# Kernel tuning notes

Hardware: AMD Instinct MI355X
Metric: run time of the kernel (lower is better)

The kernel has to match this reference:

```python
import jax, jax.numpy as jnp
import numpy as np

N_NODES = 100000
N_EDGES = 3200000
N_GRAPHS = 1024
D = 64
STEPS_PROP = 6
STEPS_S2S = 6


def setup_inputs() -> dict:
    key = jax.random.key(0)
    ks = jax.random.split(key, 16)
    inp = {}
    inp['x'] = jax.random.normal(ks[0], (N_NODES, 15), dtype=jnp.float32)
    inp['edge_index'] = jax.random.randint(ks[1], (2, N_EDGES), 0, N_NODES, dtype=jnp.int64 if jax.config.jax_enable_x64 else jnp.int32)
    inp['batch'] = jnp.sort(jax.random.randint(ks[2], (N_NODES,), 0, N_GRAPHS, dtype=jnp.int64 if jax.config.jax_enable_x64 else jnp.int32))
    s = 0.1
    inp['W0'] = jax.random.normal(ks[3], (15, D), dtype=jnp.float32) * s
    inp['b0'] = jax.random.normal(ks[4], (D,), dtype=jnp.float32) * s
    inp['Wc'] = jax.random.normal(ks[5], (D, D), dtype=jnp.float32) * s
    inp['bc'] = jax.random.normal(ks[6], (D,), dtype=jnp.float32) * s
    inp['Wih'] = jax.random.normal(ks[7], (4 * D, 2 * D), dtype=jnp.float32) * s
    inp['Whh'] = jax.random.normal(ks[8], (4 * D, D), dtype=jnp.float32) * s
    inp['bih'] = jax.random.normal(ks[9], (4 * D,), dtype=jnp.float32) * s
    inp['bhh'] = jax.random.normal(ks[10], (4 * D,), dtype=jnp.float32) * s
    inp['W1'] = jax.random.normal(ks[11], (2 * D, D), dtype=jnp.float32) * s
    inp['b1'] = jax.random.normal(ks[12], (D,), dtype=jnp.float32) * s
    inp['W2'] = jax.random.normal(ks[13], (D, 12), dtype=jnp.float32) * s
    inp['b2'] = jax.random.normal(ks[14], (12,), dtype=jnp.float32) * s
    return inp


def _gcn_forward(x, edge_index, batch, W0, b0, Wc, bc, Wih, Whh, bih, bhh, W1, b1, W2, b2):
    N = x.shape[0]
    # GCNConv normalization with self-loops (PyG semantics): A_hat = D^-1/2 (A+I) D^-1/2
    loops = jnp.arange(N, dtype=edge_index.dtype)
    row = jnp.concatenate([edge_index[0], loops])  # source
    col = jnp.concatenate([edge_index[1], loops])  # target
    deg = jax.ops.segment_sum(jnp.ones_like(col, dtype=x.dtype), col, num_segments=N)
    dinv = jnp.where(deg > 0, jax.lax.rsqrt(jnp.maximum(deg, 1e-30)), 0.0)
    norm = dinv[row] * dinv[col]  # [E+N]

    out = jax.nn.relu(x @ W0 + b0)  # [N, D]
    for _ in range(STEPS_PROP):
        h = out @ Wc  # transform first
        msg = h[row] * norm[:, None]  # gather along edges
        out = jax.nn.relu(jax.ops.segment_sum(msg, col, num_segments=N) + bc)

    # Set2Set pooling
    B = N_GRAPHS
    d = out.shape[1]
    h_l = jnp.zeros((B, d), dtype=out.dtype)
    c_l = jnp.zeros((B, d), dtype=out.dtype)
    q_star = jnp.zeros((B, 2 * d), dtype=out.dtype)
    for _ in range(STEPS_S2S):
        gates = q_star @ Wih.T + h_l @ Whh.T + bih + bhh  # [B, 4d]
        i_g, f_g, g_g, o_g = jnp.split(gates, 4, axis=1)
        c_l = jax.nn.sigmoid(f_g) * c_l + jax.nn.sigmoid(i_g) * jnp.tanh(g_g)
        h_l = jax.nn.sigmoid(o_g) * jnp.tanh(c_l)
        q = h_l  # [B, d]
        e = jnp.sum(out * q[batch], axis=-1)  # [N]
        m = jax.ops.segment_max(e, batch, num_segments=B)
        a_num = jnp.exp(e - m[batch])
        denom = jax.ops.segment_sum(a_num, batch, num_segments=B)
        a = a_num / denom[batch]
        r = jax.ops.segment_sum(a[:, None] * out, batch, num_segments=B)  # [B, d]
        q_star = jnp.concatenate([q, r], axis=-1)

    y = jax.nn.relu(q_star @ W1 + b1)
    return y @ W2 + b2  # [B, 12]


def reference(x, edge_index, batch, W0, b0, Wc, bc, Wih, Whh, bih, bhh, W1, b1, W2, b2):
    return _gcn_forward(x, edge_index, batch, W0, b0, Wc, bc, Wih, Whh, bih, bhh, W1, b1, W2, b2)
```

## Files before the change

kernel.cpp:

```cpp
#include <hip/hip_runtime.h>
#include <hip/hip_fp16.h>
#include <math.h>

#define ND 64
constexpr int BKT_SHIFT = 9;
constexpr int BKT_MASK = (1 << BKT_SHIFT) - 1;
constexpr int BCUR_PAD = 16;
constexpr int STG_TILE = 8192;
constexpr int S2S_CAP = 192;

__device__ __forceinline__ float sigmoidf_(float x){ return 1.f/(1.f+__expf(-x)); }
__device__ __forceinline__ __half2 h2lo(uint2 v){ return *reinterpret_cast<__half2*>(&v.x); }
__device__ __forceinline__ __half2 h2hi(uint2 v){ return *reinterpret_cast<__half2*>(&v.y); }
__device__ __forceinline__ __half2 shxor_h2(__half2 h, int off){
  unsigned u = *reinterpret_cast<unsigned*>(&h);
  u = __shfl_xor(u, off, 64);
  return *reinterpret_cast<__half2*>(&u);
}

__global__ void k_bhist(const int* __restrict__ col, int* __restrict__ bgcnt,
                        int E, int NBK){
  __shared__ int lhist[512];
  int t0 = blockIdx.x * STG_TILE;
  int t1 = t0 + STG_TILE; if (t1 > E) t1 = E;
  for (int i = threadIdx.x; i < NBK; i += 256) lhist[i] = 0;
  __syncthreads();
  for (int i = t0 + threadIdx.x; i < t1; i += 256)
    atomicAdd(&lhist[col[i] >> BKT_SHIFT], 1);
  __syncthreads();
  for (int i = threadIdx.x; i < NBK; i += 256)
    if (lhist[i] > 0) atomicAdd(&bgcnt[i], lhist[i]);
}

__global__ void k_bscan(const int* __restrict__ bgcnt, int* __restrict__ bstart,
                        int* __restrict__ rowptr, int NBK, int E, int N){
  __shared__ int tmp[256];
  int t = threadIdx.x;
  int v = (t < NBK) ? bgcnt[t] : 0;
  tmp[t] = v; __syncthreads();
  for (int off=1; off<256; off<<=1){
    int u = (t>=off) ? tmp[t-off] : 0;
    __syncthreads();
    tmp[t] += u;
    __syncthreads();
  }
  if (t <= NBK) bstart[t] = (t==0) ? 0 : tmp[t-1];
  if (t == 0) rowptr[N] = E;
}

__global__ void k_bcinit(const int* __restrict__ bstart, int* __restrict__ bcur, int NBK){
  int b = blockIdx.x*blockDim.x + threadIdx.x;
  if (b < NBK) bcur[b*BCUR_PAD] = bstart[b];
}

__global__ void k_stage2(const int* __restrict__ row, const int* __restrict__ col,
                         int* __restrict__ bcur, unsigned* __restrict__ pairs,
                         int E, int NBK){
  __shared__ int lhist[512];
  __shared__ int lbase[512];
  int t0 = blockIdx.x * STG_TILE;
  int t1 = t0 + STG_TILE; if (t1 > E) t1 = E;
  for (int i = threadIdx.x; i < NBK; i += 256) lhist[i] = 0;
  __syncthreads();
  for (int i = t0 + threadIdx.x; i < t1; i += 256)
    atomicAdd(&lhist[col[i] >> BKT_SHIFT], 1);
  __syncthreads();
  for (int i = threadIdx.x; i < NBK; i += 256){
    int c = lhist[i];
    lbase[i] = (c > 0) ? atomicAdd(&bcur[i*BCUR_PAD], c) : 0;
    lhist[i] = 0;
  }
  __syncthreads();
  for (int i = t0 + threadIdx.x; i < t1; i += 256){
    int d = col[i];
    int b = d >> BKT_SHIFT;
    int pos = lbase[b] + atomicAdd(&lhist[b], 1);
    pairs[pos] = ((unsigned)row[i] << BKT_SHIFT) | (unsigned)(d & BKT_MASK);
  }
}

__global__ void k_place(const unsigned* __restrict__ pairs, const int* __restrict__ bstart,
                        int* __restrict__ rowptr, float* __restrict__ dinv,
                        int* __restrict__ csr, int N){
  __shared__ int h[1 << BKT_SHIFT];
  __shared__ int excl[1 << BKT_SHIFT];
  __shared__ int tsum[256];
  int b = blockIdx.x;
  int base = b << BKT_SHIFT;
  int nend = base + (1 << BKT_SHIFT); if (nend > N) nend = N;
  int cnt = nend - base;
  int t = threadIdx.x;
  int s = bstart[b], e = bstart[b+1];

  h[2*t] = 0; h[2*t+1] = 0;
  __syncthreads();
  for (int i = s + t; i < e; i += 256)
    atomicAdd(&h[pairs[i] & BKT_MASK], 1);
  __syncthreads();
  int a0 = h[2*t], a1 = h[2*t+1];
  tsum[t] = a0 + a1;
  __syncthreads();
  for (int off=1; off<256; off<<=1){
    int u = (t>=off) ? tsum[t-off] : 0;
    __syncthreads();
    tsum[t] += u;
    __syncthreads();
  }
  int base0 = (t==0) ? 0 : tsum[t-1];
  excl[2*t]   = base0;
  excl[2*t+1] = base0 + a0;
  __syncthreads();
  for (int c = t; c < cnt; c += 256){
    int deg = h[c];
    rowptr[base + c] = s + excl[c];
    dinv[base + c] = rsqrtf((float)(deg + 1));
  }
  __syncthreads();
  for (int c = t; c < cnt; c += 256) h[c] = s + excl[c];
  __syncthreads();
  for (int i = s + t; i < e; i += 256){
    unsigned p = pairs[i];
    int pos = atomicAdd(&h[p & BKT_MASK], 1);
    csr[pos] = (int)(p >> BKT_SHIFT);
  }
}

__global__ void k_input(const float* __restrict__ x, const float* __restrict__ W0,
                        const float* __restrict__ b0, const float* __restrict__ dinv,
                        __half* __restrict__ s, int N){
  __shared__ float w0s[15*ND];
  __shared__ float b0s[ND];
  int tid = threadIdx.x;
  for (int i=tid; i<15*ND; i+=256) w0s[i] = W0[i];
  if (tid < ND) b0s[tid] = b0[tid];
  __syncthreads();
  int node = blockIdx.x*4 + (tid>>6);
  int f = tid & 63;
  if (node < N){
    float acc = b0s[f];
    const float* xr = x + (size_t)node*15;
    #pragma unroll
    for (int k=0;k<15;k++) acc += xr[k]*w0s[k*ND+f];
    s[(size_t)node*ND+f] = __float2half_rn(dinv[node]*fmaxf(acc, 0.f));
  }
}

__global__ void k_prop(const __half* __restrict__ sbuf, const int* __restrict__ rowptr,
                       const int* __restrict__ csr, const float* __restrict__ dinv,
                       const float* __restrict__ Wc, const float* __restrict__ bc,
                       __half* __restrict__ s_new, __half* __restrict__ outh,
                       int N, int wout){
  __shared__ float wcs[ND*ND];
  __shared__ float xs[16][ND];
  __shared__ float bcs[ND];
  const uint2* g8 = (const uint2*)sbuf;
  int tid = threadIdx.x;
  for (int i=tid; i<ND*ND; i+=256) wcs[i] = Wc[i];
  if (tid < ND) bcs[tid] = bc[tid];
  int nb = blockIdx.x*16;
  int wv = tid>>6, lane = tid&63;
  int grp = lane>>4, li = lane&15;

  for (int q=0; q<4; ++q){
    int node = nb + wv*4 + q;
    float val = 0.f;
    if (node < N){
      int s = rowptr[node], e = rowptr[node+1];
      __half2 z = __float2half2_rn(0.f);
      __half2 a0x=z,a0y=z, a1x=z,a1y=z, a2x=z,a2y=z, a3x=z,a3y=z;
      int i = s;
      for (; i + 16 <= e; i += 16){
        int s0 = csr[i +  0 + grp];
        int s1 = csr[i +  4 + grp];
        int s2 = csr[i +  8 + grp];
        int s3 = csr[i + 12 + grp];
        uint2 v0 = g8[(size_t)s0*16 + li];
        uint2 v1 = g8[(size_t)s1*16 + li];
        uint2 v2 = g8[(size_t)s2*16 + li];
        uint2 v3 = g8[(size_t)s3*16 + li];
        a0x = __hadd2(a0x, h2lo(v0)); a0y = __hadd2(a0y, h2hi(v0));
        a1x = __hadd2(a1x, h2lo(v1)); a1y = __hadd2(a1y, h2hi(v1));
        a2x = __hadd2(a2x, h2lo(v2)); a2y = __hadd2(a2y, h2hi(v2));
        a3x = __hadd2(a3x, h2lo(v3)); a3y = __hadd2(a3y, h2hi(v3));
      }
      for (; i + 4 <= e; i += 4){
        int s0 = csr[i + grp];
        uint2 v0 = g8[(size_t)s0*16 + li];
        a0x = __hadd2(a0x, h2lo(v0)); a0y = __hadd2(a0y, h2hi(v0));
      }
      int r = e - i;
      if (grp < r){
        int s0 = csr[i + grp];
        uint2 v0 = g8[(size_t)s0*16 + li];
        a1x = __hadd2(a1x, h2lo(v0)); a1y = __hadd2(a1y, h2hi(v0));
      }
      __half2 sxh = __hadd2(__hadd2(a0x,a1x), __hadd2(a2x,a3x));
      __half2 syh = __hadd2(__hadd2(a0y,a1y), __hadd2(a2y,a3y));
      sxh = __hadd2(sxh, shxor_h2(sxh, 16));
      syh = __hadd2(syh, shxor_h2(syh, 16));
      sxh = __hadd2(sxh, shxor_h2(sxh, 32));
      syh = __hadd2(syh, shxor_h2(syh, 32));
      uint2 sv = g8[(size_t)node*16 + li];
      sxh = __hadd2(sxh, h2lo(sv));
      syh = __hadd2(syh, h2hi(sv));
      val = (grp==0) ? __half2float(__low2half(sxh))
          : (grp==1) ? __half2float(__high2half(sxh))
          : (grp==2) ? __half2float(__low2half(syh))
          :            __half2float(__high2half(syh));
    }
    xs[wv*4+q][4*li+grp] = val;
  }
  __syncthreads();

  int f = tid&63, nq = tid>>6;
  float acc0=0.f, acc1=0.f, acc2=0.f, acc3=0.f;
  #pragma unroll 16
  for (int k=0;k<ND;k++){
    float w = wcs[k*ND+f];
    acc0 += w*xs[nq*4+0][k];
    acc1 += w*xs[nq*4+1][k];
    acc2 += w*xs[nq*4+2][k];
    acc3 += w*xs[nq*4+3][k];
  }
  int n0 = nb + nq*4;
  float bcf = bcs[f];
  #pragma unroll
  for (int j=0; j<4; ++j){
    int node = n0 + j;
    if (node < N){
      float a = (j==0)?acc0:(j==1)?acc1:(j==2)?acc2:acc3;
      float dn = dinv[node];
      float r = fmaxf(dn*a + bcf, 0.f);
      if (wout) outh[(size_t)node*ND+f] = __float2half_rn(r);
      else      s_new[(size_t)node*ND+f] = __float2half_rn(dn*r);
    }
  }
}

__global__ void k_goff(const int* __restrict__ batch, int* __restrict__ goff, int N, int B){
  int i = blockIdx.x*blockDim.x + threadIdx.x;
  if (i >= N) return;
  int b = batch[i];
  if (i == 0){ for (int g2=0; g2<=b; ++g2) goff[g2]=0; }
  else {
    int bp = batch[i-1];
    for (int g2=bp+1; g2<=b; ++g2) goff[g2]=i;
  }
  if (i == N-1){ for (int g2=b+1; g2<=B; ++g2) goff[g2]=N; }
}

__global__ void k_wprep(const float* __restrict__ Wih, const float* __restrict__ Whh,
                        const float* __restrict__ bih, const float* __restrict__ bhh,
                        float* __restrict__ WcombT, float* __restrict__ WrT,
                        float* __restrict__ bsum){
  int k = blockIdx.x;
  int j = threadIdx.x;
  WcombT[k*256 + j] = Wih[(size_t)j*128 + k] + Whh[(size_t)j*64 + k];
  WrT  [k*256 + j] = Wih[(size_t)j*128 + 64 + k];
  if (k == 0) bsum[j] = bih[j] + bhh[j];
}

__global__ void k_s2s(const __half* __restrict__ nodef, const int* __restrict__ goff,
                      const float* __restrict__ WcombT, const float* __restrict__ WrT,
                      const float* __restrict__ bsum,
                      const float* __restrict__ W1, const float* __restrict__ b1,
                      const float* __restrict__ W2, const float* __restrict__ b2,
                      float* __restrict__ outy, int B){
  __shared__ float qsr[128];
  __shared__ float clr[64];
  __shared__ float gat[256];
  __shared__ float redm[16], redd[16];
  __shared__ float redr[16][64];
  __shared__ float yy[64];
  extern __shared__ uint2 snode[];
  int tid = threadIdx.x;
  int g = blockIdx.x;
  if (g >= B) return;
  if (tid < 128) qsr[tid] = 0.f;
  if (tid < 64)  clr[tid] = 0.f;
  int lane = tid&63, wv = tid>>6;
  int grp = lane>>4, li = lane&15;
  int gidx = wv*4 + grp;
  int s = goff[g], e = goff[g+1];
  int cnt = e - s;
  const uint2* nf = (const uint2*)nodef;
  bool lds_ok = (cnt <= S2S_CAP);
  if (lds_ok){
    for (int i = tid; i < cnt*16; i += 256){
      int n = i >> 4, c = i & 15;
      snode[n*17 + c] = nf[(size_t)(s+n)*16 + c];
    }
  }
  __syncthreads();

  for (int step=0; step<6; ++step){
    {
      float a0 = bsum[tid], a1 = 0.f;
      for (int k=0; k<64; k+=2){
        a0 += WcombT[(k  )*256+tid]*qsr[k  ] + WrT[(k  )*256+tid]*qsr[64+k  ];
        a1 += WcombT[(k+1)*256+tid]*qsr[k+1] + WrT[(k+1)*256+tid]*qsr[64+k+1];
      }
      gat[tid] = a0 + a1;
    }
    __syncthreads();
    if (tid < 64){
      float ig = sigmoidf_(gat[tid]);
      float fg = sigmoidf_(gat[64+tid]);
      float gv = tanhf(gat[128+tid]);
      float og = sigmoidf_(gat[192+tid]);
      float c = fg*clr[tid] + ig*gv;
      float h = og*tanhf(c);
      clr[tid] = c;
      qsr[tid] = h;
    }
    __syncthreads();
    {
      float4 q4 = *(const float4*)&qsr[4*li];
      float m = -3.0e38f, denom = 0.f;
      float r0=0.f, r1=0.f, r2=0.f, r3=0.f;
      if (lds_ok){
        for (int n = gidx; n < cnt; n += 16){
          uint2 v = snode[n*17 + li];
          float2 flo = __half22float2(h2lo(v));
          float2 fhi = __half22float2(h2hi(v));
          float p = flo.x*q4.x + flo.y*q4.y + fhi.x*q4.z + fhi.y*q4.w;
          p += __shfl_xor(p, 1, 64);
          p += __shfl_xor(p, 2, 64);
          p += __shfl_xor(p, 4, 64);
          p += __shfl_xor(p, 8, 64);
          if (p > m){
            float sc = __expf(m - p);
            denom *= sc; r0 *= sc; r1 *= sc; r2 *= sc; r3 *= sc;
            m = p;
          }
          float w = __expf(p - m);
          denom += w;
          r0 += w*flo.x; r1 += w*flo.y; r2 += w*fhi.x; r3 += w*fhi.y;
        }
      } else {
        for (int n = s + gidx; n < e; n += 16){
          uint2 v = nf[(size_t)n*16 + li];
          float2 flo = __half22float2(h2lo(v));
          float2 fhi = __half22float2(h2hi(v));
          float p = flo.x*q4.x + flo.y*q4.y + fhi.x*q4.z + fhi.y*q4.w;
          p += __shfl_xor(p, 1, 64);
          p += __shfl_xor(p, 2, 64);
          p += __shfl_xor(p, 4, 64);
          p += __shfl_xor(p, 8, 64);
          if (p > m){
            float sc = __expf(m - p);
            denom *= sc; r0 *= sc; r1 *= sc; r2 *= sc; r3 *= sc;
            m = p;
          }
          float w = __expf(p - m);
          denom += w;
          r0 += w*flo.x; r1 += w*flo.y; r2 += w*fhi.x; r3 += w*fhi.y;
        }
      }
      if (li == 0){ redm[gidx] = m; redd[gidx] = denom; }
      redr[gidx][4*li+0] = r0;
      redr[gidx][4*li+1] = r1;
      redr[gidx][4*li+2] = r2;
      redr[gidx][4*li+3] = r3;
    }
    __syncthreads();
    if (tid < 64){
      float mm = -3.0e38f;
      #pragma unroll
      for (int k=0;k<16;k++) mm = fmaxf(mm, redm[k]);
      float dt = 0.f, rs = 0.f;
      #pragma unroll
      for (int k=0;k<16;k++){
        float sc = __expf(redm[k] - mm);
        dt += redd[k]*sc;
        rs += redr[k][tid]*sc;
      }
      qsr[64+tid] = (dt > 0.f) ? rs/dt : 0.f;
    }
    __syncthreads();
  }
  if (tid < 64){
    float acc = b1[tid];
    for (int k=0;k<128;k++) acc += qsr[k]*W1[k*64+tid];
    yy[tid] = fmaxf(acc, 0.f);
  }
  __syncthreads();
  if (tid < 12){
    float a2 = b2[tid];
    for (int k=0;k<64;k++) a2 += yy[k]*W2[k*12+tid];
    outy[(size_t)g*12+tid] = a2;
  }
}

extern "C" void kernel_launch(void* const* d_in, const int* in_sizes, int n_in,
                              void* d_out, int out_size, void* d_ws, size_t ws_size,
                              hipStream_t stream){
  const float* x    = (const float*)d_in[0];
  const int*   ei   = (const int*)d_in[1];
  const int*   batch= (const int*)d_in[2];
  const float* W0   = (const float*)d_in[3];
  const float* b0   = (const float*)d_in[4];
  const float* Wc   = (const float*)d_in[5];
  const float* bc   = (const float*)d_in[6];
  const float* Wih  = (const float*)d_in[7];
  const float* Whh  = (const float*)d_in[8];
  const float* bih  = (const float*)d_in[9];
  const float* bhh  = (const float*)d_in[10];
  const float* W1   = (const float*)d_in[11];
  const float* b1   = (const float*)d_in[12];
  const float* W2   = (const float*)d_in[13];
  const float* b2   = (const float*)d_in[14];
  float* yout = (float*)d_out;

  const int N = in_sizes[0]/15;
  const int E = in_sizes[1]/2;
  const int B = out_size/12;
  const int NBK = (N + (1<<BKT_SHIFT) - 1) >> BKT_SHIFT;
  const int* row = ei;
  const int* col = ei + E;

  char* ws = (char*)d_ws;
  size_t off = 0;
  auto alloc = [&](size_t bytes)->void*{
    void* p = ws + off; off = (off + bytes + 255) & ~(size_t)255; return p;
  };
  int*      bgcnt   = (int*)     alloc((size_t)(NBK+1)*4);
  int*      bstart  = (int*)     alloc((size_t)(NBK+1)*4);
  int*      bcur    = (int*)     alloc((size_t)NBK*BCUR_PAD*4);
  int*      rowptr  = (int*)     alloc((size_t)(N+1)*4);
  unsigned* pairs   = (unsigned*)alloc((size_t)E*4);
  int*      csr     = (int*)     alloc((size_t)E*4);
  float*    dinv    = (float*)   alloc((size_t)N*4);
  __half*   nodef   = (__half*)  alloc((size_t)N*ND*2);
  __half*   s_a     = (__half*)  alloc((size_t)N*ND*2);
  __half*   s_b     = (__half*)  alloc((size_t)N*ND*2);
  int*      goff    = (int*)     alloc((size_t)(B+1)*4);
  float*    WcombT  = (float*)   alloc(64*256*4);
  float*    WrT     = (float*)   alloc(64*256*4);
  float*    bsum    = (float*)   alloc(256*4);
  (void)ws_size; (void)n_in;

  hipMemsetAsync(bgcnt, 0, (size_t)(NBK+1)*4, stream);

  int nstg = (E + STG_TILE - 1)/STG_TILE;
  k_bhist <<<nstg, 256, 0, stream>>>(col, bgcnt, E, NBK);
  k_bscan <<<1, 256, 0, stream>>>(bgcnt, bstart, rowptr, NBK, E, N);
  k_bcinit<<<(NBK+255)/256, 256, 0, stream>>>(bstart, bcur, NBK);
  k_stage2<<<nstg, 256, 0, stream>>>(row, col, bcur, pairs, E, NBK);
  k_place <<<NBK, 256, 0, stream>>>(pairs, bstart, rowptr, dinv, csr, N);

  k_input<<<(N+3)/4, 256, 0, stream>>>(x, W0, b0, dinv, s_a, N);
  __half* scur = s_a; __half* snxt = s_b;
  for (int s6=0; s6<6; ++s6){
    k_prop<<<(N+15)/16, 256, 0, stream>>>(scur, rowptr, csr, dinv,
                                          Wc, bc, snxt, nodef, N, (s6==5)?1:0);
    __half* t = scur; scur = snxt; snxt = t;
  }

  k_goff<<<(N+255)/256, 256, 0, stream>>>(batch, goff, N, B);
  k_wprep<<<64, 256, 0, stream>>>(Wih, Whh, bih, bhh, WcombT, WrT, bsum);
  size_t s2s_lds = (size_t)S2S_CAP*17*sizeof(uint2);
  k_s2s<<<B, 256, s2s_lds, stream>>>(nodef, goff, WcombT, WrT, bsum,
                                     W1, b1, W2, b2, yout, B);
}
```

Baseline: 854.6 us.

## Batch four graphs per Set2Set block with fp16 LSTM weights staged in LDS

The Set2Set kernel now handles four graphs per 256-thread block, with one wavefront per graph for the attention pass. It stages the LSTM weights, prepacked as half2, into LDS once per block so that each weight element is reused across four graphs. The LDS node cache shrinks to 144 nodes per graph. Weight traffic and block count go down, but gate weights lose fp16 precision. Each graph gets only one wave for attention, larger graphs spill to the global path, and the high LDS use may cut occupancy.

```diff
diff --git a/kernel.cpp b/kernel.cpp
--- a/kernel.cpp
+++ b/kernel.cpp
@@ -7,7 +7,7 @@
 constexpr int BKT_MASK = (1 << BKT_SHIFT) - 1;
 constexpr int BCUR_PAD = 16;
 constexpr int STG_TILE = 8192;
-constexpr int S2S_CAP = 192;
+constexpr int S2S_CAP = 144;
 
 __device__ __forceinline__ float sigmoidf_(float x){ return 1.f/(1.f+__expf(-x)); }
 __device__ __forceinline__ __half2 h2lo(uint2 v){ return *reinterpret_cast<__half2*>(&v.x); }
@@ -251,76 +251,108 @@
 
 __global__ void k_wprep(const float* __restrict__ Wih, const float* __restrict__ Whh,
                         const float* __restrict__ bih, const float* __restrict__ bhh,
-                        float* __restrict__ WcombT, float* __restrict__ WrT,
+                        unsigned* __restrict__ WC2, unsigned* __restrict__ WR2,
                         float* __restrict__ bsum){
-  int k = blockIdx.x;
-  int j = threadIdx.x;
-  WcombT[k*256 + j] = Wih[(size_t)j*128 + k] + Whh[(size_t)j*64 + k];
-  WrT  [k*256 + j] = Wih[(size_t)j*128 + 64 + k];
-  if (k == 0) bsum[j] = bih[j] + bhh[j];
+  int k2 = blockIdx.x;
+  int j  = threadIdx.x;
+  int k = 2*k2;
+  float c0 = Wih[(size_t)j*128 + k]     + Whh[(size_t)j*64 + k];
+  float c1 = Wih[(size_t)j*128 + k + 1] + Whh[(size_t)j*64 + k + 1];
+  float r0 = Wih[(size_t)j*128 + 64 + k];
+  float r1 = Wih[(size_t)j*128 + 64 + k + 1];
+  __half2 hc = __halves2half2(__float2half_rn(c0), __float2half_rn(c1));
+  __half2 hr = __halves2half2(__float2half_rn(r0), __float2half_rn(r1));
+  WC2[k2*256 + j] = *reinterpret_cast<unsigned*>(&hc);
+  WR2[k2*256 + j] = *reinterpret_cast<unsigned*>(&hr);
+  if (k2 == 0) bsum[j] = bih[j] + bhh[j];
 }
 
 __global__ void k_s2s(const __half* __restrict__ nodef, const int* __restrict__ goff,
-                      const float* __restrict__ WcombT, const float* __restrict__ WrT,
+                      const unsigned* __restrict__ WC2g, const unsigned* __restrict__ WR2g,
                       const float* __restrict__ bsum,
                       const float* __restrict__ W1, const float* __restrict__ b1,
                       const float* __restrict__ W2, const float* __restrict__ b2,
                       float* __restrict__ outy, int B){
-  __shared__ float qsr[128];
-  __shared__ float clr[64];
-  __shared__ float gat[256];
-  __shared__ float redm[16], redd[16];
-  __shared__ float redr[16][64];
-  __shared__ float yy[64];
-  extern __shared__ uint2 snode[];
+  __shared__ unsigned lwc[32*256];
+  __shared__ unsigned lwr[32*256];
+  __shared__ float qsr[4][128];
+  __shared__ float clr[4][64];
+  __shared__ float gat[4][256];
+  __shared__ float redm[4][4], redd[4][4];
+  __shared__ float redr[4][4][64];
+  __shared__ float yy[4][64];
+  __shared__ uint2 snode[4][S2S_CAP*17];
+
   int tid = threadIdx.x;
-  int g = blockIdx.x;
-  if (g >= B) return;
-  if (tid < 128) qsr[tid] = 0.f;
-  if (tid < 64)  clr[tid] = 0.f;
+  int g0 = blockIdx.x*4;
   int lane = tid&63, wv = tid>>6;
   int grp = lane>>4, li = lane&15;
-  int gidx = wv*4 + grp;
-  int s = goff[g], e = goff[g+1];
-  int cnt = e - s;
+
+  for (int i=tid; i<32*256; i+=256){ lwc[i] = WC2g[i]; lwr[i] = WR2g[i]; }
+  for (int i=tid; i<4*128; i+=256) qsr[i>>7][i&127] = 0.f;
+  if (tid < 256){ clr[tid>>6][tid&63] = 0.f; }
+
+  int mygraph = g0 + wv;
+  int s = 0, cnt = 0;
   const uint2* nf = (const uint2*)nodef;
-  bool lds_ok = (cnt <= S2S_CAP);
-  if (lds_ok){
-    for (int i = tid; i < cnt*16; i += 256){
-      int n = i >> 4, c = i & 15;
-      snode[n*17 + c] = nf[(size_t)(s+n)*16 + c];
-    }
-  }
+  bool lds_ok = false;
+  if (mygraph < B){
+    s = goff[mygraph];
+    cnt = goff[mygraph+1] - s;
+    lds_ok = (cnt <= S2S_CAP);
+    if (lds_ok){
+      for (int i = lane; i < cnt*16; i += 64){
+        int n = i >> 4, c = i & 15;
+        snode[wv][n*17 + c] = nf[(size_t)(s+n)*16 + c];
+      }
+    }
+  }
+  float bsv = bsum[tid];
   __syncthreads();
 
   for (int step=0; step<6; ++step){
     {
-      float a0 = bsum[tid], a1 = 0.f;
-      for (int k=0; k<64; k+=2){
-        a0 += WcombT[(k  )*256+tid]*qsr[k  ] + WrT[(k  )*256+tid]*qsr[64+k  ];
-        a1 += WcombT[(k+1)*256+tid]*qsr[k+1] + WrT[(k+1)*256+tid]*qsr[64+k+1];
-      }
-      gat[tid] = a0 + a1;
-    }
-    __syncthreads();
-    if (tid < 64){
-      float ig = sigmoidf_(gat[tid]);
-      float fg = sigmoidf_(gat[64+tid]);
-      float gv = tanhf(gat[128+tid]);
-      float og = sigmoidf_(gat[192+tid]);
-      float c = fg*clr[tid] + ig*gv;
+      float a0=bsv, a1=bsv, a2=bsv, a3=bsv;
+      for (int k2=0; k2<32; ++k2){
+        unsigned uc = lwc[k2*256 + tid];
+        unsigned ur = lwr[k2*256 + tid];
+        float2 wc = __half22float2(*reinterpret_cast<__half2*>(&uc));
+        float2 wr = __half22float2(*reinterpret_cast<__half2*>(&ur));
+        float2 h0 = *(const float2*)&qsr[0][2*k2];
+        float2 h1 = *(const float2*)&qsr[1][2*k2];
+        float2 h2 = *(const float2*)&qsr[2][2*k2];
+        float2 h3 = *(const float2*)&qsr[3][2*k2];
+        float2 r0 = *(const float2*)&qsr[0][64+2*k2];
+        float2 r1 = *(const float2*)&qsr[1][64+2*k2];
+        float2 r2 = *(const float2*)&qsr[2][64+2*k2];
+        float2 r3 = *(const float2*)&qsr[3][64+2*k2];
+        a0 += wc.x*h0.x + wc.y*h0.y + wr.x*r0.x + wr.y*r0.y;
+        a1 += wc.x*h1.x + wc.y*h1.y + wr.x*r1.x + wr.y*r1.y;
+        a2 += wc.x*h2.x + wc.y*h2.y + wr.x*r2.x + wr.y*r2.y;
+        a3 += wc.x*h3.x + wc.y*h3.y + wr.x*r3.x + wr.y*r3.y;
+      }
+      gat[0][tid]=a0; gat[1][tid]=a1; gat[2][tid]=a2; gat[3][tid]=a3;
+    }
+    __syncthreads();
+    {
+      int gg = tid>>6, d = tid&63;
+      float ig = sigmoidf_(gat[gg][d]);
+      float fg = sigmoidf_(gat[gg][64+d]);
+      float gv = tanhf(gat[gg][128+d]);
+      float og = sigmoidf_(gat[gg][192+d]);
+      float c = fg*clr[gg][d] + ig*gv;
       float h = og*tanhf(c);
-      clr[tid] = c;
-      qsr[tid] = h;
+      clr[gg][d] = c;
+      qsr[gg][d] = h;
     }
     __syncthreads();
     {
-      float4 q4 = *(const float4*)&qsr[4*li];
+      float4 q4 = *(const float4*)&qsr[wv][4*li];
       float m = -3.0e38f, denom = 0.f;
       float r0=0.f, r1=0.f, r2=0.f, r3=0.f;
       if (lds_ok){
-        for (int n = gidx; n < cnt; n += 16){
-          uint2 v = snode[n*17 + li];
+        for (int n = grp; n < cnt; n += 4){
+          uint2 v = snode[wv][n*17 + li];
           float2 flo = __half22float2(h2lo(v));
           float2 fhi = __half22float2(h2hi(v));
           float p = flo.x*q4.x + flo.y*q4.y + fhi.x*q4.z + fhi.y*q4.w;
@@ -337,9 +369,9 @@
           denom += w;
           r0 += w*flo.x; r1 += w*flo.y; r2 += w*fhi.x; r3 += w*fhi.y;
         }
-      } else {
-        for (int n = s + gidx; n < e; n += 16){
-          uint2 v = nf[(size_t)n*16 + li];
+      } else if (mygraph < B){
+        for (int n = grp; n < cnt; n += 4){
+          uint2 v = nf[(size_t)(s+n)*16 + li];
           float2 flo = __half22float2(h2lo(v));
           float2 fhi = __half22float2(h2hi(v));
           float p = flo.x*q4.x + flo.y*q4.y + fhi.x*q4.z + fhi.y*q4.w;
@@ -357,38 +389,38 @@
           r0 += w*flo.x; r1 += w*flo.y; r2 += w*fhi.x; r3 += w*fhi.y;
         }
       }
-      if (li == 0){ redm[gidx] = m; redd[gidx] = denom; }
-      redr[gidx][4*li+0] = r0;
-      redr[gidx][4*li+1] = r1;
-      redr[gidx][4*li+2] = r2;
-      redr[gidx][4*li+3] = r3;
-    }
-    __syncthreads();
-    if (tid < 64){
-      float mm = -3.0e38f;
-      #pragma unroll
-      for (int k=0;k<16;k++) mm = fmaxf(mm, redm[k]);
-      float dt = 0.f, rs = 0.f;
-      #pragma unroll
-      for (int k=0;k<16;k++){
-        float sc = __expf(redm[k] - mm);
-        dt += redd[k]*sc;
-        rs += redr[k][tid]*sc;
-      }
-      qsr[64+tid] = (dt > 0.f) ? rs/dt : 0.f;
-    }
-    __syncthreads();
-  }
-  if (tid < 64){
-    float acc = b1[tid];
-    for (int k=0;k<128;k++) acc += qsr[k]*W1[k*64+tid];
-    yy[tid] = fmaxf(acc, 0.f);
-  }
-  __syncthreads();
-  if (tid < 12){
-    float a2 = b2[tid];
-    for (int k=0;k<64;k++) a2 += yy[k]*W2[k*12+tid];
-    outy[(size_t)g*12+tid] = a2;
+      if (li == 0){ redm[wv][grp] = m; redd[wv][grp] = denom; }
+      redr[wv][grp][4*li+0] = r0;
+      redr[wv][grp][4*li+1] = r1;
+      redr[wv][grp][4*li+2] = r2;
+      redr[wv][grp][4*li+3] = r3;
+    }
+    __syncthreads();
+    {
+      int gg = tid>>6, d = tid&63;
+      float m0=redm[gg][0], m1=redm[gg][1], m2=redm[gg][2], m3=redm[gg][3];
+      float mm = fmaxf(fmaxf(m0,m1), fmaxf(m2,m3));
+      float s0=__expf(m0-mm), s1=__expf(m1-mm), s2=__expf(m2-mm), s3=__expf(m3-mm);
+      float dt = redd[gg][0]*s0 + redd[gg][1]*s1 + redd[gg][2]*s2 + redd[gg][3]*s3;
+      float rs = redr[gg][0][d]*s0 + redr[gg][1][d]*s1 + redr[gg][2][d]*s2 + redr[gg][3][d]*s3;
+      qsr[gg][64+d] = (dt > 0.f) ? rs/dt : 0.f;
+    }
+    __syncthreads();
+  }
+  {
+    int gg = tid>>6, f = tid&63;
+    float acc = b1[f];
+    for (int k=0;k<128;k++) acc += qsr[gg][k]*W1[k*64+f];
+    yy[gg][f] = fmaxf(acc, 0.f);
+  }
+  __syncthreads();
+  if (tid < 48){
+    int gg = tid/12, o = tid%12;
+    if (g0+gg < B){
+      float a2 = b2[o];
+      for (int k=0;k<64;k++) a2 += yy[gg][k]*W2[k*12+o];
+      outy[(size_t)(g0+gg)*12+o] = a2;
+    }
   }
 }
 
@@ -435,8 +467,8 @@
   __half*   s_a     = (__half*)  alloc((size_t)N*ND*2);
   __half*   s_b     = (__half*)  alloc((size_t)N*ND*2);
   int*      goff    = (int*)     alloc((size_t)(B+1)*4);
-  float*    WcombT  = (float*)   alloc(64*256*4);
-  float*    WrT     = (float*)   alloc(64*256*4);
+  unsigned* WC2     = (unsigned*)alloc(32*256*4);
+  unsigned* WR2     = (unsigned*)alloc(32*256*4);
   float*    bsum    = (float*)   alloc(256*4);
   (void)ws_size; (void)n_in;
 
@@ -458,8 +490,7 @@
   }
 
   k_goff<<<(N+255)/256, 256, 0, stream>>>(batch, goff, N, B);
-  k_wprep<<<64, 256, 0, stream>>>(Wih, Whh, bih, bhh, WcombT, WrT, bsum);
-  size_t s2s_lds = (size_t)S2S_CAP*17*sizeof(uint2);
-  k_s2s<<<B, 256, s2s_lds, stream>>>(nodef, goff, WcombT, WrT, bsum,
+  k_wprep<<<32, 256, 0, stream>>>(Wih, Whh, bih, bhh, WC2, WR2, bsum);
+  k_s2s<<<(B+3)/4, 256, 0, stream>>>(nodef, goff, WC2, WR2, bsum,
                                      W1, b1, W2, b2, yout, B);
 }
```

Measured after the change: 839.1 us. No clear change (-1.8%).
